# Performance work log

Hardware: AMD Instinct MI355X
Metric: run time of the kernel (lower is better)

## Reference

```python
import jax, jax.numpy as jnp
import numpy as np

B, C, H, W = 4, 192, 128, 128
EQK, EV, HEADS = 192, 192, 8


def setup_inputs() -> dict:
    key = jax.random.key(0)
    ks = jax.random.split(key, 11)
    s = 0.02
    return {
        "q": jax.random.normal(ks[0], (B, C, H, W), jnp.float32),
        "k": jax.random.normal(ks[1], (B, C, H, W), jnp.float32),
        "v": jax.random.normal(ks[2], (B, C, H, W), jnp.float32),
        "Wq": jax.random.normal(ks[3], (EQK, C), jnp.float32) * s,
        "bq": jax.random.normal(ks[4], (EQK,), jnp.float32) * s,
        "Wk": jax.random.normal(ks[5], (EQK, C), jnp.float32) * s,
        "bk": jax.random.normal(ks[6], (EQK,), jnp.float32) * s,
        "Wv": jax.random.normal(ks[7], (EV, C), jnp.float32) * s,
        "bv": jax.random.normal(ks[8], (EV,), jnp.float32) * s,
        "Wo": jax.random.normal(ks[9], (C, EV), jnp.float32) * s,
        "bo": jax.random.normal(ks[10], (C,), jnp.float32) * s,
    }


def reference(q, k, v, Wq, bq, Wk, bk, Wv, bv, Wo, bo):
    b, c, h, w = q.shape
    n = h * w
    d_qk, d_v = EQK // HEADS, EV // HEADS

    def proj(x, Wt, bt, e):
        # 1x1 conv == per-pixel matmul; flatten spatial dims to n tokens
        return (jnp.einsum('oc,bchw->bohw', Wt, x) + bt[None, :, None, None]).reshape(b, e, n)

    # [b, heads, d, n] head split (embed splits contiguously into H*d, matching torch reshape)
    qh = proj(q, Wq, bq, EQK).reshape(b, HEADS, d_qk, n)
    kh = proj(k, Wk, bk, EQK).reshape(b, HEADS, d_qk, n)
    vh = proj(v, Wv, bv, EV).reshape(b, HEADS, d_v, n)

    qh = jax.nn.softmax(qh, axis=2)  # softmax over feature dim d_qk (torch dim=1 on [bh,d,n])
    kh = jax.nn.softmax(kh, axis=3)  # softmax over token dim n   (torch dim=2 on [bh,d,n])

    # linear attention: context = K @ V^T -> [b, H, d_qk, d_v]; then context^T @ Q
    ctx = jnp.einsum('bhdn,bhen->bhde', kh, vh)
    yh = jnp.einsum('bhde,bhdn->bhen', ctx, qh)  # [b, H, d_v, n]

    y = yh.reshape(b, EV, h, w)
    out = jnp.einsum('oc,bchw->bohw', Wo, y) + bo[None, :, None, None]
    return out
```

## Files before the change

kernel.cpp:

```cpp
#include <hip/hip_runtime.h>

#define CC 192
#define NN 16384
#define XST 198
#define QST 200

typedef unsigned short u16;
typedef __attribute__((ext_vector_type(4))) float f32x4;
typedef __attribute__((ext_vector_type(8))) __bf16 bf16x8;
typedef __attribute__((ext_vector_type(8))) u16 u16x8;
typedef __attribute__((ext_vector_type(4))) u16 u16x4;

union FragU { u16x8 u; bf16x8 b; };

__device__ __forceinline__ u16 f2bf(float f) {
  union { float f; unsigned u; } x; x.f = f;
  return (u16)((x.u + 0x7FFFu + ((x.u >> 16) & 1u)) >> 16);
}
__device__ __forceinline__ float bf2f(u16 h) {
  union { unsigned u; float f; } x; x.u = ((unsigned)h) << 16;
  return x.f;
}

__global__ __launch_bounds__(256, 2)
void kproj(const float* __restrict__ k, const float* __restrict__ v,
           const u16* __restrict__ Wb, const float* __restrict__ bk,
           const float* __restrict__ bv, u16* __restrict__ Sexp,
           u16* __restrict__ Vbuf)
{
  __shared__ __align__(16) u16 Xs[64][XST];
  const int b = blockIdx.y, pj = blockIdx.z;
  const int t0 = blockIdx.x * 64;
  const int tid = threadIdx.x;
  const int lg = (tid >> 4) & 3, lc = tid & 15;
  const int wave = tid >> 6, e0 = wave * 48;
  const int tg = tid & 15, chq = tid >> 4;

  const float* xb = (pj ? v : k) + (size_t)b * CC * NN;
  const u16* Wp = Wb + (pj ? 2 : 1) * 36864;
  const float* bias = pj ? bv : bk;
  u16* outp = pj ? Vbuf : Sexp;

  f32x4 p[12];
#pragma unroll
  for (int i = 0; i < 12; ++i)
    p[i] = *reinterpret_cast<const f32x4*>(xb + (size_t)(i * 16 + chq) * NN + t0 + tg * 4);

  FragU wfr[6][3];
#pragma unroll
  for (int ks = 0; ks < 6; ++ks)
#pragma unroll
    for (int et = 0; et < 3; ++et)
      wfr[ks][et].u = *reinterpret_cast<const u16x8*>(
          &Wp[(e0 + et * 16 + lc) * 192 + ks * 32 + lg * 8]);

#pragma unroll
  for (int i = 0; i < 12; ++i) {
    const int ch = i * 16 + chq;
    Xs[tg * 4 + 0][ch] = f2bf(p[i][0]);
    Xs[tg * 4 + 1][ch] = f2bf(p[i][1]);
    Xs[tg * 4 + 2][ch] = f2bf(p[i][2]);
    Xs[tg * 4 + 3][ch] = f2bf(p[i][3]);
  }
  __syncthreads();

  f32x4 acc[3][4];
#pragma unroll
  for (int et = 0; et < 3; ++et)
#pragma unroll
    for (int nt = 0; nt < 4; ++nt) acc[et][nt] = f32x4{0.f, 0.f, 0.f, 0.f};

#pragma unroll
  for (int ks = 0; ks < 6; ++ks) {
    FragU bb[4];
#pragma unroll
    for (int nt = 0; nt < 4; ++nt)
      bb[nt].u = *reinterpret_cast<const u16x8*>(&Xs[nt * 16 + lc][ks * 32 + lg * 8]);
#pragma unroll
    for (int et = 0; et < 3; ++et)
#pragma unroll
      for (int nt = 0; nt < 4; ++nt)
        acc[et][nt] = __builtin_amdgcn_mfma_f32_16x16x32_bf16(wfr[ks][et].b, bb[nt].b,
                                                             acc[et][nt], 0, 0, 0);
  }

#pragma unroll
  for (int et = 0; et < 3; ++et)
#pragma unroll
    for (int r = 0; r < 4; ++r) {
      const int e = e0 + et * 16 + lg * 4 + r;
      const float bb = bias[e];
      u16* orow = outp + (size_t)(b * 192 + e) * NN + t0;
#pragma unroll
      for (int nt = 0; nt < 4; ++nt) {
        float val = acc[et][nt][r] + bb;
        if (!pj) val = __expf(val);
        orow[nt * 16 + lc] = f2bf(val);
      }
    }
}

__global__ __launch_bounds__(512, 2)
void kctx(const u16* __restrict__ Sexp, const u16* __restrict__ Vbuf,
          float* __restrict__ part)
{
  const int b = blockIdx.y, slab = blockIdx.x;
  const int tid = threadIdx.x;
  const int h = tid >> 6;
  const int lg = (tid >> 4) & 3, lc = tid & 15;
  const int n0 = slab * 128;
  const size_t basee = (size_t)b * 192 * NN;

  f32x4 cacc[2][2];
#pragma unroll
  for (int mt = 0; mt < 2; ++mt)
#pragma unroll
    for (int nt = 0; nt < 2; ++nt) cacc[mt][nt] = f32x4{0.f, 0.f, 0.f, 0.f};

#pragma unroll
  for (int ks = 0; ks < 4; ++ks) {
    const int tok = n0 + ks * 32 + lg * 8;
    FragU av[2], bs[2];
#pragma unroll
    for (int mt = 0; mt < 2; ++mt) {
      int row = h * 24 + mt * 16 + lc;
      if (row > 191) row = 191;
      av[mt].u = *reinterpret_cast<const u16x8*>(&Vbuf[basee + (size_t)row * NN + tok]);
      bs[mt].u = *reinterpret_cast<const u16x8*>(&Sexp[basee + (size_t)row * NN + tok]);
    }
#pragma unroll
    for (int mt = 0; mt < 2; ++mt)
#pragma unroll
      for (int nt = 0; nt < 2; ++nt)
        cacc[mt][nt] = __builtin_amdgcn_mfma_f32_16x16x32_bf16(
            av[mt].b, bs[nt].b, cacc[mt][nt], 0, 0, 0);
  }

  float* pp = part + (((size_t)(b * 128 + slab)) * 8 + h) * 576;
#pragma unroll
  for (int mt = 0; mt < 2; ++mt)
#pragma unroll
    for (int nt = 0; nt < 2; ++nt)
#pragma unroll
      for (int r = 0; r < 4; ++r) {
        const int dv = mt * 16 + lg * 4 + r;
        const int d = nt * 16 + lc;
        if (dv < 24 && d < 24) pp[dv * 24 + d] = cacc[mt][nt][r];
      }
}

__global__ __launch_bounds__(256, 2)
void krow(const u16* __restrict__ Sexp, float* __restrict__ ksum)
{
  __shared__ float red[4];
  const int row = blockIdx.x;
  const int tid = threadIdx.x;
  const u16* p = Sexp + (size_t)row * NN;
  float s = 0.f;
#pragma unroll
  for (int i = 0; i < 8; ++i) {
    u16x8 vv = *reinterpret_cast<const u16x8*>(&p[(i * 256 + tid) * 8]);
#pragma unroll
    for (int j = 0; j < 8; ++j) s += bf2f(vv[j]);
  }
#pragma unroll
  for (int off = 1; off < 64; off <<= 1) s += __shfl_xor(s, off);
  if ((tid & 63) == 0) red[tid >> 6] = s;
  __syncthreads();
  if (tid == 0) ksum[row] = red[0] + red[1] + red[2] + red[3];
}

__global__ void kr2(const float* __restrict__ part, const float* __restrict__ ksum,
                    float* __restrict__ ctx)
{
  const int idx = blockIdx.x * 256 + threadIdx.x;
  if (idx >= 4608) return;
  const int b = blockIdx.y;
  const int h = idx / 576, rem = idx % 576;
  const int d = rem % 24;
  float s = 0.f;
  const float* pp = part + (size_t)b * 128 * 4608 + idx;
#pragma unroll 8
  for (int j = 0; j < 128; ++j) s += pp[(size_t)j * 4608];
  ctx[(size_t)b * 4608 + idx] = s / ksum[b * 192 + h * 24 + d];
}

__global__ void km(const float* __restrict__ Wo, const float* __restrict__ ctx,
                   u16* __restrict__ Meff)
{
  const int o = blockIdx.x, b = blockIdx.y, j = threadIdx.x;
  const int h = j / 24, d = j % 24;
  const float* Wrow = Wo + o * 192 + h * 24;
  const float* crow = ctx + (size_t)b * 4608 + h * 576 + d;
  float acc = 0.f;
#pragma unroll
  for (int dv = 0; dv < 24; ++dv) acc += Wrow[dv] * crow[dv * 24];
  Meff[(b * 192 + o) * 192 + j] = f2bf(acc);
}

__global__ __launch_bounds__(256, 2)
void kq(const float* __restrict__ q, const u16* __restrict__ Wb,
        const float* __restrict__ bq, const u16* __restrict__ Meff,
        const float* __restrict__ bo, float* __restrict__ out)
{
  __shared__ __align__(16) u16 Xs[64][XST];
  __shared__ __align__(16) u16 SsT[64][QST];

  const int b = blockIdx.y;
  const int t0 = blockIdx.x * 64;
  const int tid = threadIdx.x;
  const int lg = (tid >> 4) & 3, lc = tid & 15;
  const int wave = tid >> 6, e0 = wave * 48;
  const int tg = tid & 15, chq = tid >> 4;
  const u16* Mb = Meff + b * 36864;

  f32x4 p[12];
  const float* xb = q + (size_t)b * CC * NN;
#pragma unroll
  for (int i = 0; i < 12; ++i)
    p[i] = *reinterpret_cast<const f32x4*>(xb + (size_t)(i * 16 + chq) * NN + t0 + tg * 4);

  FragU wfr[6][3];
#pragma unroll
  for (int ks = 0; ks < 6; ++ks)
#pragma unroll
    for (int et = 0; et < 3; ++et)
      wfr[ks][et].u = *reinterpret_cast<const u16x8*>(
          &Wb[(e0 + et * 16 + lc) * 192 + ks * 32 + lg * 8]);

#pragma unroll
  for (int i = 0; i < 12; ++i) {
    const int ch = i * 16 + chq;
    Xs[tg * 4 + 0][ch] = f2bf(p[i][0]);
    Xs[tg * 4 + 1][ch] = f2bf(p[i][1]);
    Xs[tg * 4 + 2][ch] = f2bf(p[i][2]);
    Xs[tg * 4 + 3][ch] = f2bf(p[i][3]);
  }
  __syncthreads();

  f32x4 acc[3][4];
#pragma unroll
  for (int et = 0; et < 3; ++et)
#pragma unroll
    for (int nt = 0; nt < 4; ++nt) acc[et][nt] = f32x4{0.f, 0.f, 0.f, 0.f};
#pragma unroll
  for (int ks = 0; ks < 6; ++ks) {
    FragU bb[4];
#pragma unroll
    for (int nt = 0; nt < 4; ++nt)
      bb[nt].u = *reinterpret_cast<const u16x8*>(&Xs[nt * 16 + lc][ks * 32 + lg * 8]);
#pragma unroll
    for (int et = 0; et < 3; ++et)
#pragma unroll
      for (int nt = 0; nt < 4; ++nt)
        acc[et][nt] = __builtin_amdgcn_mfma_f32_16x16x32_bf16(wfr[ks][et].b, bb[nt].b,
                                                             acc[et][nt], 0, 0, 0);
  }

#pragma unroll
  for (int et = 0; et < 3; ++et)
#pragma unroll
    for (int r = 0; r < 4; ++r) {
      const int e = e0 + et * 16 + lg * 4 + r;
      const float bias = bq[e];
#pragma unroll
      for (int nt = 0; nt < 4; ++nt)
        SsT[nt * 16 + lc][e] = f2bf(acc[et][nt][r] + bias);
    }
  __syncthreads();

#pragma unroll
  for (int ii = 0; ii < 2; ++ii) {
    const int item = ii * 256 + tid;
    const int n = item & 63, h = item >> 6;
    u16* rowp = &SsT[n][h * 24];
    float vals[24];
    float m = -1e30f;
#pragma unroll
    for (int d = 0; d < 24; ++d) {
      vals[d] = bf2f(rowp[d]);
      m = fmaxf(m, vals[d]);
    }
    float s = 0.f;
#pragma unroll
    for (int d = 0; d < 24; ++d) { vals[d] = __expf(vals[d] - m); s += vals[d]; }
    const float inv = 1.f / s;
#pragma unroll
    for (int d = 0; d < 24; ++d) rowp[d] = f2bf(vals[d] * inv);
  }
  __syncthreads();

#pragma unroll
  for (int et = 0; et < 3; ++et)
#pragma unroll
    for (int nt = 0; nt < 4; ++nt) acc[et][nt] = f32x4{0.f, 0.f, 0.f, 0.f};
#pragma unroll
  for (int ks = 0; ks < 6; ++ks) {
    FragU a[3], bb[4];
#pragma unroll
    for (int et = 0; et < 3; ++et)
      a[et].u = *reinterpret_cast<const u16x8*>(
          &Mb[(e0 + et * 16 + lc) * 192 + ks * 32 + lg * 8]);
#pragma unroll
    for (int nt = 0; nt < 4; ++nt)
      bb[nt].u = *reinterpret_cast<const u16x8*>(&SsT[nt * 16 + lc][ks * 32 + lg * 8]);
#pragma unroll
    for (int et = 0; et < 3; ++et)
#pragma unroll
      for (int nt = 0; nt < 4; ++nt)
        acc[et][nt] = __builtin_amdgcn_mfma_f32_16x16x32_bf16(a[et].b, bb[nt].b,
                                                             acc[et][nt], 0, 0, 0);
  }

#pragma unroll
  for (int et = 0; et < 3; ++et)
#pragma unroll
    for (int r = 0; r < 4; ++r) {
      const int row = e0 + et * 16 + lg * 4 + r;
      const float bias = bo[row];
#pragma unroll
      for (int nt = 0; nt < 4; ++nt)
        out[(size_t)(b * 192 + row) * NN + t0 + nt * 16 + lc] = acc[et][nt][r] + bias;
    }
}

__global__ void kz(const float* __restrict__ Wq, const float* __restrict__ Wk,
                   const float* __restrict__ Wv, u16* __restrict__ Wb)
{
  const int i = blockIdx.x * 256 + threadIdx.x;
  if (i < 110592) {
    const float* src = (i < 36864) ? Wq : (i < 73728) ? Wk : Wv;
    Wb[i] = f2bf(src[i % 36864]);
  }
}

extern "C" void kernel_launch(void* const* d_in, const int* in_sizes, int n_in,
                              void* d_out, int out_size, void* d_ws, size_t ws_size,
                              hipStream_t stream)
{
  const float* q  = (const float*)d_in[0];
  const float* k  = (const float*)d_in[1];
  const float* v  = (const float*)d_in[2];
  const float* Wq = (const float*)d_in[3];
  const float* bq = (const float*)d_in[4];
  const float* Wk = (const float*)d_in[5];
  const float* bk = (const float*)d_in[6];
  const float* Wv = (const float*)d_in[7];
  const float* bv = (const float*)d_in[8];
  const float* Wo = (const float*)d_in[9];
  const float* bo = (const float*)d_in[10];
  float* out = (float*)d_out;

  char* w = (char*)d_ws;
  u16*   Wb   = (u16*)(w);
  u16*   Sexp = (u16*)(w + 221184);
  u16*   Vbuf = (u16*)(w + 25387008);
  float* part = (float*)(w + 50552832);
  float* ksum = (float*)(w + 59990016);
  float* ctx  = (float*)(w + 59993088);
  u16*   Meff = (u16*)(w + 60066816);

  hipLaunchKernelGGL(kz, dim3(432), dim3(256), 0, stream, Wq, Wk, Wv, Wb);
  hipLaunchKernelGGL(kproj, dim3(256, 4, 2), dim3(256), 0, stream,
                     k, v, Wb, bk, bv, Sexp, Vbuf);
  hipLaunchKernelGGL(krow, dim3(768), dim3(256), 0, stream, Sexp, ksum);
  hipLaunchKernelGGL(kctx, dim3(128, 4), dim3(512), 0, stream, Sexp, Vbuf, part);
  hipLaunchKernelGGL(kr2, dim3(18, 4), dim3(256), 0, stream, part, ksum, ctx);
  hipLaunchKernelGGL(km, dim3(192, 4), dim3(192), 0, stream, Wo, ctx, Meff);
  hipLaunchKernelGGL(kq, dim3(256, 4), dim3(256), 0, stream, q, Wb, bq, Meff, bo, out);
}
```

Baseline: 103.2 us.

## Stage input tiles via global_load_lds DMA as fp32, convert to bf16 on read

```diff
diff --git a/kernel.cpp b/kernel.cpp
--- a/kernel.cpp
+++ b/kernel.cpp
@@ -2,14 +2,13 @@
 
 #define CC 192
 #define NN 16384
-#define XST 198
+#define QSD 264
 #define QST 200
 
 typedef unsigned short u16;
 typedef __attribute__((ext_vector_type(4))) float f32x4;
 typedef __attribute__((ext_vector_type(8))) __bf16 bf16x8;
 typedef __attribute__((ext_vector_type(8))) u16 u16x8;
-typedef __attribute__((ext_vector_type(4))) u16 u16x4;
 
 union FragU { u16x8 u; bf16x8 b; };
 
@@ -20,6 +19,32 @@
 __device__ __forceinline__ float bf2f(u16 h) {
   union { unsigned u; float f; } x; x.u = ((unsigned)h) << 16;
   return x.f;
+}
+
+__device__ __forceinline__ void gl_lds16(const float* g, float* l) {
+  __builtin_amdgcn_global_load_lds(
+      (const __attribute__((address_space(1))) void*)g,
+      (__attribute__((address_space(3))) void*)l, 16, 0, 0);
+}
+
+__device__ __forceinline__ void stage_dma(const float* __restrict__ xb, int t0,
+                                          int lane, int wv, float* Xf) {
+#pragma unroll
+  for (int i = 0; i < 12; ++i) {
+    const int q = wv * 12 + i;
+    const float* gsrc = xb + (size_t)(q * 4 + (lane >> 4)) * NN + t0 + (lane & 15) * 4;
+    gl_lds16(gsrc, &Xf[q * QSD]);
+  }
+}
+
+__device__ __forceinline__ u16x8 bfrag(const float* Xf, int ks, int nt, int lg, int lc) {
+  u16x8 f;
+#pragma unroll
+  for (int j = 0; j < 8; ++j) {
+    const int ch = ks * 32 + lg * 8 + j;
+    f[j] = f2bf(Xf[(ch >> 2) * QSD + (ch & 3) * 64 + nt * 16 + lc]);
+  }
+  return f;
 }
 
 __global__ __launch_bounds__(256, 2)
@@ -28,23 +53,20 @@
            const float* __restrict__ bv, u16* __restrict__ Sexp,
            u16* __restrict__ Vbuf)
 {
-  __shared__ __align__(16) u16 Xs[64][XST];
+  __shared__ __align__(16) float Xf[48 * QSD];
   const int b = blockIdx.y, pj = blockIdx.z;
   const int t0 = blockIdx.x * 64;
   const int tid = threadIdx.x;
-  const int lg = (tid >> 4) & 3, lc = tid & 15;
-  const int wave = tid >> 6, e0 = wave * 48;
-  const int tg = tid & 15, chq = tid >> 4;
+  const int lane = tid & 63, wv = tid >> 6;
+  const int lg = lane >> 4, lc = lane & 15;
+  const int e0 = wv * 48;
 
   const float* xb = (pj ? v : k) + (size_t)b * CC * NN;
   const u16* Wp = Wb + (pj ? 2 : 1) * 36864;
   const float* bias = pj ? bv : bk;
   u16* outp = pj ? Vbuf : Sexp;
 
-  f32x4 p[12];
-#pragma unroll
-  for (int i = 0; i < 12; ++i)
-    p[i] = *reinterpret_cast<const f32x4*>(xb + (size_t)(i * 16 + chq) * NN + t0 + tg * 4);
+  stage_dma(xb, t0, lane, wv, Xf);
 
   FragU wfr[6][3];
 #pragma unroll
@@ -54,14 +76,6 @@
       wfr[ks][et].u = *reinterpret_cast<const u16x8*>(
           &Wp[(e0 + et * 16 + lc) * 192 + ks * 32 + lg * 8]);
 
-#pragma unroll
-  for (int i = 0; i < 12; ++i) {
-    const int ch = i * 16 + chq;
-    Xs[tg * 4 + 0][ch] = f2bf(p[i][0]);
-    Xs[tg * 4 + 1][ch] = f2bf(p[i][1]);
-    Xs[tg * 4 + 2][ch] = f2bf(p[i][2]);
-    Xs[tg * 4 + 3][ch] = f2bf(p[i][3]);
-  }
   __syncthreads();
 
   f32x4 acc[3][4];
@@ -74,8 +88,7 @@
   for (int ks = 0; ks < 6; ++ks) {
     FragU bb[4];
 #pragma unroll
-    for (int nt = 0; nt < 4; ++nt)
-      bb[nt].u = *reinterpret_cast<const u16x8*>(&Xs[nt * 16 + lc][ks * 32 + lg * 8]);
+    for (int nt = 0; nt < 4; ++nt) bb[nt].u = bfrag(Xf, ks, nt, lg, lc);
 #pragma unroll
     for (int et = 0; et < 3; ++et)
 #pragma unroll
@@ -203,22 +216,18 @@
         const float* __restrict__ bq, const u16* __restrict__ Meff,
         const float* __restrict__ bo, float* __restrict__ out)
 {
-  __shared__ __align__(16) u16 Xs[64][XST];
+  __shared__ __align__(16) float Xf[48 * QSD];
   __shared__ __align__(16) u16 SsT[64][QST];
 
   const int b = blockIdx.y;
   const int t0 = blockIdx.x * 64;
   const int tid = threadIdx.x;
-  const int lg = (tid >> 4) & 3, lc = tid & 15;
-  const int wave = tid >> 6, e0 = wave * 48;
-  const int tg = tid & 15, chq = tid >> 4;
+  const int lane = tid & 63, wv = tid >> 6;
+  const int lg = lane >> 4, lc = lane & 15;
+  const int e0 = wv * 48;
   const u16* Mb = Meff + b * 36864;
 
-  f32x4 p[12];
-  const float* xb = q + (size_t)b * CC * NN;
-#pragma unroll
-  for (int i = 0; i < 12; ++i)
-    p[i] = *reinterpret_cast<const f32x4*>(xb + (size_t)(i * 16 + chq) * NN + t0 + tg * 4);
+  stage_dma(q + (size_t)b * CC * NN, t0, lane, wv, Xf);
 
   FragU wfr[6][3];
 #pragma unroll
@@ -228,14 +237,6 @@
       wfr[ks][et].u = *reinterpret_cast<const u16x8*>(
           &Wb[(e0 + et * 16 + lc) * 192 + ks * 32 + lg * 8]);
 
-#pragma unroll
-  for (int i = 0; i < 12; ++i) {
-    const int ch = i * 16 + chq;
-    Xs[tg * 4 + 0][ch] = f2bf(p[i][0]);
-    Xs[tg * 4 + 1][ch] = f2bf(p[i][1]);
-    Xs[tg * 4 + 2][ch] = f2bf(p[i][2]);
-    Xs[tg * 4 + 3][ch] = f2bf(p[i][3]);
-  }
   __syncthreads();
 
   f32x4 acc[3][4];
@@ -247,8 +248,7 @@
   for (int ks = 0; ks < 6; ++ks) {
     FragU bb[4];
 #pragma unroll
-    for (int nt = 0; nt < 4; ++nt)
-      bb[nt].u = *reinterpret_cast<const u16x8*>(&Xs[nt * 16 + lc][ks * 32 + lg * 8]);
+    for (int nt = 0; nt < 4; ++nt) bb[nt].u = bfrag(Xf, ks, nt, lg, lc);
 #pragma unroll
     for (int et = 0; et < 3; ++et)
 #pragma unroll
```

Measured after the change: 110.0 us. 1.07x slower.
